# Performance work log

Measured on AMD Instinct MI355X. Metric: run time of the kernel, lower is better.

The kernel has to match this reference:

```python
import jax, jax.numpy as jnp
import numpy as np

# DH-SFNN: 2 dendritic LIF layers (denri, no tanh, reset-by-subtraction) + leaky readout integrator.
GAMMA = 0.5   # surrogate gradient scale
LENS = 0.5    # surrogate gradient width
VTH = 1.0     # spike threshold
DT = 1.0

@jax.custom_vjp
def spike_fn(x):
    # Heaviside forward, Gaussian surrogate backward (act_fun_adp)
    return (x > 0.0).astype(x.dtype)

def _spike_fwd(x):
    return spike_fn(x), x

def _spike_bwd(x, g):
    sg = GAMMA * jnp.exp(-x * x / (2.0 * LENS * LENS)) / (jnp.sqrt(2.0 * jnp.pi) * LENS)
    return (g * sg,)

spike_fn.defvjp(_spike_fwd, _spike_bwd)

B, T, IN, H, O, K = 256, 250, 700, 256, 20, 4  # batch, time, in_dim, hidden, out_dim, branch
WARMUP = 10


def _branch_mask(rng, out_dim, in_dim, k):
    # Each neuron's k branches see a disjoint random partition of the inputs.
    m = np.zeros((out_dim * k, in_dim), np.float32)
    step = in_dim // k
    for i in range(out_dim):
        perm = rng.permutation(in_dim)
        for j in range(k):
            m[i * k + j, perm[j * step:(j + 1) * step]] = 1.0
    return m


def setup_inputs() -> dict:
    key = jax.random.key(0)
    ks = jax.random.split(key, 12)
    rng = np.random.default_rng(0)
    s1 = 1.0 / np.sqrt(IN)
    s2 = 1.0 / np.sqrt(H)
    # branch-masked dense weights (apply_mask() already baked in)
    W1 = jax.random.uniform(ks[0], (H * K, IN), minval=-s1, maxval=s1) * jnp.asarray(_branch_mask(rng, H, IN, K))
    b1 = jax.random.uniform(ks[1], (H * K,), minval=-s1, maxval=s1)
    tau_n1 = jax.random.uniform(ks[2], (H, K), minval=2.0, maxval=6.0)
    tau_m1 = jax.random.uniform(ks[3], (H,), minval=0.0, maxval=4.0)
    W2 = jax.random.uniform(ks[4], (H * K, H), minval=-s2, maxval=s2) * jnp.asarray(_branch_mask(rng, H, H, K))
    b2 = jax.random.uniform(ks[5], (H * K,), minval=-s2, maxval=s2)
    tau_n2 = jax.random.uniform(ks[6], (H, K), minval=2.0, maxval=6.0)
    tau_m2 = jax.random.uniform(ks[7], (H,), minval=0.0, maxval=4.0)
    Wr = jax.random.uniform(ks[8], (O, H), minval=-s2, maxval=s2)
    br = jax.random.uniform(ks[9], (O,), minval=-s2, maxval=s2)
    tau_mr = jax.random.uniform(ks[10], (O,), minval=0.0, maxval=4.0)
    # sparse binary spike train input (SHD-like)
    x = (jax.random.uniform(ks[11], (B, T, IN)) < 0.1).astype(jnp.float32)
    return dict(x=x, W1=W1, b1=b1, tau_n1=tau_n1, tau_m1=tau_m1,
                W2=W2, b2=b2, tau_n2=tau_n2, tau_m2=tau_m2,
                Wr=Wr, br=br, tau_mr=tau_mr, warmup=WARMUP)


def reference(x, W1, b1, tau_n1, tau_m1, W2, b2, tau_n2, tau_m2, Wr, br, tau_mr, warmup):
    Bb, Tt, _ = x.shape
    beta1 = jax.nn.sigmoid(tau_n1)   # [H,K] dendritic decay
    alpha1 = jax.nn.sigmoid(tau_m1)  # [H]   soma decay
    beta2 = jax.nn.sigmoid(tau_n2)
    alpha2 = jax.nn.sigmoid(tau_m2)
    alphar = jax.nn.sigmoid(tau_mr)  # [O]

    def dense_branch(inp, W, b):
        return (inp @ W.T + b).reshape(inp.shape[0], -1, K)  # [B,H,K]

    def step(carry, xt):
        d1, m1, s1, d2, m2, s2, mr, acc, t = carry
        # layer 1: dendritic filtering then LIF with soft reset
        d1 = beta1 * d1 + (1.0 - beta1) * dense_branch(xt, W1, b1)
        m1 = m1 * alpha1 + (1.0 - alpha1) * DT * d1.sum(-1) - VTH * s1
        s1 = spike_fn(m1 - VTH)
        # layer 2
        d2 = beta2 * d2 + (1.0 - beta2) * dense_branch(s1, W2, b2)
        m2 = m2 * alpha2 + (1.0 - alpha2) * DT * d2.sum(-1) - VTH * s2
        s2 = spike_fn(m2 - VTH)
        # leaky readout integrator
        mr = mr * alphar + (1.0 - alphar) * (s2 @ Wr.T + br)
        acc = acc + jnp.where(t >= warmup, mr, jnp.zeros_like(mr))
        return (d1, m1, s1, d2, m2, s2, mr, acc, t + 1), None

    z = lambda *s: jnp.zeros(s, x.dtype)
    carry0 = (z(Bb, H, K), z(Bb, H), z(Bb, H),
              z(Bb, H, K), z(Bb, H), z(Bb, H),
              z(Bb, O), z(Bb, O), jnp.int32(0))
    carry, _ = jax.lax.scan(step, carry0, jnp.moveaxis(x, 1, 0))
    acc = carry[7]
    return acc / (Tt - warmup)  # readout_mode == 'mean'
```

## Files before the change

### kernel.cpp

```cpp
#include <hip/hip_runtime.h>
#include <hip/hip_bf16.h>

typedef unsigned short us16;
typedef unsigned int u32;
typedef unsigned long long ull;

#define B_   256
#define T_   250
#define IN_  700
#define KP_  704
#define H_   256
#define O_   20
#define HK_  1024
#define NPAIR_ (B_ * T_)
#define LDP_ 40
#define CP_  136

typedef __attribute__((ext_vector_type(8))) short short8;
typedef __attribute__((ext_vector_type(4))) float f32x4;

__device__ __forceinline__ float bfbits(unsigned int lo16) {
    union { unsigned int i; float f; } v; v.i = lo16 << 16; return v.f;
}
__device__ __forceinline__ float bflo(unsigned int u) {
    union { unsigned int i; float f; } v; v.i = u << 16; return v.f;
}
__device__ __forceinline__ float bfhi(unsigned int u) {
    union { unsigned int i; float f; } v; v.i = u & 0xffff0000u; return v.f;
}
__device__ __forceinline__ us16 f2bfu(float f) {
    __hip_bfloat16 h = __float2bfloat16(f);
    union { __hip_bfloat16 h; us16 u; } c; c.h = h; return c.u;
}
__device__ __forceinline__ float sigm(float x) { return 1.0f / (1.0f + expf(-x)); }
__device__ __forceinline__ int rfl(int v) { return __builtin_amdgcn_readfirstlane(v); }

__device__ __forceinline__ bool detect_bf16(const us16* __restrict__ taun) {
    int ok = 0;
#pragma unroll
    for (int i = 0; i < 8; i += 2) ok += ((taun[i] >> 8) == 0x40) ? 1 : 0;
    return ok == 4;
}
__device__ __forceinline__ float ldany(const void* __restrict__ p, long i, bool isb) {
    return isb ? bfbits(((const us16*)p)[i]) : ((const float*)p)[i];
}

__device__ __forceinline__ void async_cp16(const us16* g, us16* l) {
    __builtin_amdgcn_global_load_lds(
        (const __attribute__((address_space(1))) u32*)g,
        (__attribute__((address_space(3))) u32*)l, 16, 0, 0);
}

__global__ __launch_bounds__(256) void cvt_rows2(
    const void* __restrict__ xin, const void* __restrict__ w1in,
    us16* __restrict__ xout, us16* __restrict__ w1out,
    const us16* __restrict__ taun) {
    const bool isb = detect_bf16(taun);
    const int r = blockIdx.x * 4 + (threadIdx.x >> 6);
    const int l = threadIdx.x & 63;
    const void* in; us16* out; long ibase, obase;
    if (r < NPAIR_) {
        in = xin;  out = xout;  ibase = (long)r * IN_; obase = (long)r * KP_;
    } else {
        const int r2 = r - NPAIR_;
        if (r2 >= HK_) return;
        in = w1in; out = w1out; ibase = (long)r2 * IN_; obase = (long)r2 * KP_;
    }
    for (int c = l; c < 88; c += 64) {
        uint4 o;
        if (c < 87) {
            if (isb) {
                uint2 lo = *(const uint2*)((const us16*)in + ibase + 8 * c);
                uint2 hi = *(const uint2*)((const us16*)in + ibase + 8 * c + 4);
                o.x = lo.x; o.y = lo.y; o.z = hi.x; o.w = hi.y;
            } else {
                float4 f0 = *(const float4*)((const float*)in + ibase + 8 * c);
                float4 f1 = *(const float4*)((const float*)in + ibase + 8 * c + 4);
                o.x = (u32)f2bfu(f0.x) | ((u32)f2bfu(f0.y) << 16);
                o.y = (u32)f2bfu(f0.z) | ((u32)f2bfu(f0.w) << 16);
                o.z = (u32)f2bfu(f1.x) | ((u32)f2bfu(f1.y) << 16);
                o.w = (u32)f2bfu(f1.z) | ((u32)f2bfu(f1.w) << 16);
            }
        } else {
            o.z = 0u; o.w = 0u;
            if (isb) {
                uint2 lo = *(const uint2*)((const us16*)in + ibase + 696);
                o.x = lo.x; o.y = lo.y;
            } else {
                float4 f0 = *(const float4*)((const float*)in + ibase + 696);
                o.x = (u32)f2bfu(f0.x) | ((u32)f2bfu(f0.y) << 16);
                o.y = (u32)f2bfu(f0.z) | ((u32)f2bfu(f0.w) << 16);
            }
        }
        *(uint4*)(out + obase + 8 * c) = o;
    }
}

__global__ void transpose_to_bf16(const void* __restrict__ in, us16* __restrict__ out,
                                  int R, int C, const us16* __restrict__ taun) {
    const bool isb = detect_bf16(taun);
    __shared__ us16 tile[32][33];
    int c0 = blockIdx.x * 32, r0 = blockIdx.y * 32;
    int tx = threadIdx.x, ty = threadIdx.y;
#pragma unroll
    for (int j = 0; j < 32; j += 8) {
        int r = r0 + ty + j, c = c0 + tx;
        if (r < R && c < C) tile[ty + j][tx] = f2bfu(ldany(in, (long)r * C + c, isb));
    }
    __syncthreads();
#pragma unroll
    for (int j = 0; j < 32; j += 8) {
        int c = c0 + ty + j, r = r0 + tx;
        if (c < C && r < R) out[(long)c * R + r] = tile[tx][ty + j];
    }
}

__global__ __launch_bounds__(256) void gemm_bf(
    const us16* __restrict__ Xb, const us16* __restrict__ W1b,
    us16* __restrict__ Apre)
{
    __shared__ __align__(16) us16 smem[32768];

    const int L  = blockIdx.x;
    const int mt = (L & 7) + ((L >> 6) << 3);
    const int nt = (L >> 3) & 7;
    if (mt >= NPAIR_ / 128) return;
    const int m0 = mt * 128, n0 = nt * 128;

    const int tid  = threadIdx.x;
    const int lane = tid & 63;
    const int w    = tid >> 6;
    const int wr   = w >> 1, wc = w & 1;
    const int l16  = lane & 15, quad = lane >> 4;

    const int rr    = lane >> 3;
    const int ccsw  = ((lane & 7) ^ rr) * 8;
    const us16* xg[4]; const us16* wg[4];
    int asl[4], bsl[4];
#pragma unroll
    for (int i = 0; i < 4; ++i) {
        const int blkrow = (w * 4 + i) * 8;
        xg[i]  = Xb  + (long)(m0 + blkrow + rr) * KP_ + ccsw;
        wg[i]  = W1b + (long)(n0 + blkrow + rr) * KP_ + ccsw;
        asl[i] = (w * 4 + i) * 512;
        bsl[i] = 8192 + (w * 4 + i) * 512;
    }

    f32x4 acc[4][4];
#pragma unroll
    for (int i = 0; i < 4; ++i)
#pragma unroll
        for (int j = 0; j < 4; ++j) acc[i][j] = (f32x4){0.f, 0.f, 0.f, 0.f};

    const int sw = l16 & 7;
    int aoff0[4], aoff1[4], boff0[4], boff1[4];
#pragma unroll
    for (int i = 0; i < 4; ++i) {
        const int ar = wr * 64 + i * 16 + l16;
        const int br = wc * 64 + i * 16 + l16;
        aoff0[i] = ar * 64 + ((quad ^ sw) << 3);
        aoff1[i] = ar * 64 + (((quad + 4) ^ sw) << 3);
        boff0[i] = 8192 + br * 64 + ((quad ^ sw) << 3);
        boff1[i] = 8192 + br * 64 + (((quad + 4) ^ sw) << 3);
    }

#pragma unroll
    for (int i = 0; i < 4; ++i) async_cp16(xg[i], smem + asl[i]);
#pragma unroll
    for (int i = 0; i < 4; ++i) async_cp16(wg[i], smem + bsl[i]);
    __syncthreads();

    for (int s = 0; s < 11; ++s) {
        const int cur = (s & 1) * 16384;
        const int nxt = 16384 - cur;
        if (s + 1 < 11) {
            const int kb = (s + 1) * 64;
#pragma unroll
            for (int i = 0; i < 4; ++i) async_cp16(xg[i] + kb, smem + nxt + asl[i]);
#pragma unroll
            for (int i = 0; i < 4; ++i) async_cp16(wg[i] + kb, smem + nxt + bsl[i]);
        }

        short8 af[4][2], bfv[4][2];
#pragma unroll
        for (int i = 0; i < 4; ++i) {
            af[i][0]  = *(const short8*)(smem + cur + aoff0[i]);
            af[i][1]  = *(const short8*)(smem + cur + aoff1[i]);
            bfv[i][0] = *(const short8*)(smem + cur + boff0[i]);
            bfv[i][1] = *(const short8*)(smem + cur + boff1[i]);
        }
#pragma unroll
        for (int h = 0; h < 2; ++h)
#pragma unroll
            for (int i = 0; i < 4; ++i)
#pragma unroll
                for (int j = 0; j < 4; ++j)
                    acc[i][j] = __builtin_amdgcn_mfma_f32_16x16x32_bf16(
                        af[i][h], bfv[j][h], acc[i][j], 0, 0, 0);

        __syncthreads();
    }

#pragma unroll
    for (int i = 0; i < 4; ++i)
#pragma unroll
        for (int j = 0; j < 4; ++j)
#pragma unroll
            for (int r = 0; r < 4; ++r)
                smem[(wr * 64 + i * 16 + quad * 4 + r) * CP_ +
                     (wc * 64 + j * 16 + l16)] = f2bfu(acc[i][j][r]);
    __syncthreads();
    {
        const int c8 = (lane & 15) * 8;
#pragma unroll
        for (int r2 = 0; r2 < 8; ++r2) {
            const int row = w * 32 + r2 * 4 + (lane >> 4);
            const uint4 v = *(const uint4*)(smem + row * CP_ + c8);
            *(uint4*)(Apre + (long)(m0 + row) * HK_ + n0 + c8) = v;
        }
    }
}

__device__ void wave_recur(
    const us16* __restrict__ Apre,
    const void* __restrict__ b1,  const void* __restrict__ tau_n1,
    const void* __restrict__ tau_m1,
    const void* __restrict__ b2,  const void* __restrict__ tau_n2,
    const void* __restrict__ tau_m2,
    const void* __restrict__ Wr,  const void* __restrict__ br,
    const void* __restrict__ tau_mr,
    const us16* __restrict__ W2T,
    int wu, bool isb, int b, int lane,
    void* __restrict__ out)
{
    float be1[16], cb1[16], be2[16], cb2[16], d1[16], d2[16];
#pragma unroll
    for (int e = 0; e < 16; ++e) {
        const long gi = (long)lane * 16 + e;
        const float t1 = sigm(ldany(tau_n1, gi, isb));
        be1[e] = t1; cb1[e] = (1.f - t1) * ldany(b1, gi, isb);
        const float t2 = sigm(ldany(tau_n2, gi, isb));
        be2[e] = t2; cb2[e] = (1.f - t2) * ldany(b2, gi, isb);
        d1[e] = 0.f; d2[e] = 0.f;
    }
    float al1[4], al2[4], m1[4], s1[4], m2[4], s2[4];
#pragma unroll
    for (int j = 0; j < 4; ++j) {
        al1[j] = sigm(ldany(tau_m1, lane * 4 + j, isb));
        al2[j] = sigm(ldany(tau_m2, lane * 4 + j, isb));
        m1[j] = 0.f; s1[j] = 0.f; m2[j] = 0.f; s2[j] = 0.f;
    }
    float alr = 0.f, brv = 0.f;
    if (lane < O_) { alr = sigm(ldany(tau_mr, lane, isb)); brv = ldany(br, lane, isb); }
    float mrv = 0.f, accO = 0.f;

    const us16* ap = Apre + (long)b * T_ * HK_ + lane * 16;

    auto wstep = [&](int t, uint4 lo, uint4 hi) {
        float a[16];
        a[0]=bflo(lo.x);  a[1]=bfhi(lo.x);  a[2]=bflo(lo.y);  a[3]=bfhi(lo.y);
        a[4]=bflo(lo.z);  a[5]=bfhi(lo.z);  a[6]=bflo(lo.w);  a[7]=bfhi(lo.w);
        a[8]=bflo(hi.x);  a[9]=bfhi(hi.x);  a[10]=bflo(hi.y); a[11]=bfhi(hi.y);
        a[12]=bflo(hi.z); a[13]=bfhi(hi.z); a[14]=bflo(hi.w); a[15]=bfhi(hi.w);
#pragma unroll
        for (int e = 0; e < 16; ++e)
            d1[e] = be1[e] * d1[e] + cb1[e] + (1.f - be1[e]) * a[e];
        unsigned long long bal1[4];
#pragma unroll
        for (int j = 0; j < 4; ++j) {
            const float s = (d1[j*4+0] + d1[j*4+1]) + (d1[j*4+2] + d1[j*4+3]);
            m1[j] = m1[j] * al1[j] + (1.f - al1[j]) * s - s1[j];
            s1[j] = (m1[j] > 1.0f) ? 1.f : 0.f;
            bal1[j] = __ballot(s1[j] > 0.f);
        }
        if ((bal1[0] | bal1[1] | bal1[2] | bal1[3]) != 0ull) {
            float g[16];
#pragma unroll
            for (int e = 0; e < 16; ++e) g[e] = 0.f;
            for (int j2 = 0; j2 < 4; ++j2) {
                unsigned long long mm = bal1[j2];
                while (mm) {
                    const int i = __ffsll(mm) - 1; mm &= mm - 1;
                    const us16* wv = W2T + ((long)(i * 4 + j2) << 10) + lane * 16;
                    const uint4 wl = *(const uint4*)wv;
                    const uint4 wh = *(const uint4*)(wv + 8);
                    g[0]+=bflo(wl.x);  g[1]+=bfhi(wl.x);  g[2]+=bflo(wl.y);  g[3]+=bfhi(wl.y);
                    g[4]+=bflo(wl.z);  g[5]+=bfhi(wl.z);  g[6]+=bflo(wl.w);  g[7]+=bfhi(wl.w);
                    g[8]+=bflo(wh.x);  g[9]+=bfhi(wh.x);  g[10]+=bflo(wh.y); g[11]+=bfhi(wh.y);
                    g[12]+=bflo(wh.z); g[13]+=bfhi(wh.z); g[14]+=bflo(wh.w); g[15]+=bfhi(wh.w);
                }
            }
#pragma unroll
            for (int e = 0; e < 16; ++e)
                d2[e] = be2[e] * d2[e] + cb2[e] + (1.f - be2[e]) * g[e];
        } else {
#pragma unroll
            for (int e = 0; e < 16; ++e)
                d2[e] = be2[e] * d2[e] + cb2[e];
        }
        unsigned long long bal2[4];
#pragma unroll
        for (int j = 0; j < 4; ++j) {
            const float s = (d2[j*4+0] + d2[j*4+1]) + (d2[j*4+2] + d2[j*4+3]);
            m2[j] = m2[j] * al2[j] + (1.f - al2[j]) * s - s2[j];
            s2[j] = (m2[j] > 1.0f) ? 1.f : 0.f;
            bal2[j] = __ballot(s2[j] > 0.f);
        }
        if (lane < O_) {
            float sum = brv;
            if ((bal2[0] | bal2[1] | bal2[2] | bal2[3]) != 0ull) {
                for (int j2 = 0; j2 < 4; ++j2) {
                    unsigned long long mm = bal2[j2];
                    while (mm) {
                        const int i = __ffsll(mm) - 1; mm &= mm - 1;
                        sum += ldany(Wr, (long)lane * H_ + (i * 4 + j2), isb);
                    }
                }
            }
            mrv = alr * mrv + (1.f - alr) * sum;
            if (t >= wu) accO += mrv;
        }
    };

    uint4 q0a = *(const uint4*)(ap);
    uint4 q0b = *(const uint4*)(ap + 8);
    uint4 q1a = *(const uint4*)(ap + HK_);
    uint4 q1b = *(const uint4*)(ap + HK_ + 8);
    uint4 q2a = *(const uint4*)(ap + 2 * HK_);
    uint4 q2b = *(const uint4*)(ap + 2 * HK_ + 8);
    uint4 q3a = *(const uint4*)(ap + 3 * HK_);
    uint4 q3b = *(const uint4*)(ap + 3 * HK_ + 8);

    int t = 0;
    for (int it = 0; it < 62; ++it) {
        wstep(t + 0, q0a, q0b);
        q0a = *(const uint4*)(ap + (long)(t + 4) * HK_);
        q0b = *(const uint4*)(ap + (long)(t + 4) * HK_ + 8);
        wstep(t + 1, q1a, q1b);
        if (t + 5 < T_) {
            q1a = *(const uint4*)(ap + (long)(t + 5) * HK_);
            q1b = *(const uint4*)(ap + (long)(t + 5) * HK_ + 8);
        }
        wstep(t + 2, q2a, q2b);
        if (t + 6 < T_) {
            q2a = *(const uint4*)(ap + (long)(t + 6) * HK_);
            q2b = *(const uint4*)(ap + (long)(t + 6) * HK_ + 8);
        }
        wstep(t + 3, q3a, q3b);
        if (t + 7 < T_) {
            q3a = *(const uint4*)(ap + (long)(t + 7) * HK_);
            q3b = *(const uint4*)(ap + (long)(t + 7) * HK_ + 8);
        }
        t += 4;
    }
    wstep(248, q0a, q0b);
    wstep(249, q1a, q1b);

    if (lane < O_) {
        const float res = accO / (float)(T_ - wu);
        if (isb) ((us16*)out)[b * O_ + lane] = f2bfu(res);
        else     ((float*)out)[b * O_ + lane] = res;
    }
}

__global__ __launch_bounds__(256) void l1_check(
    const us16* __restrict__ Apre,
    const void* __restrict__ b1,  const void* __restrict__ tau_n1,
    const void* __restrict__ tau_m1,
    const void* __restrict__ b2,  const void* __restrict__ tau_n2,
    const void* __restrict__ tau_m2,
    const void* __restrict__ Wr,  const void* __restrict__ br,
    const void* __restrict__ tau_mr,
    const int* __restrict__ warmup_p,
    int* __restrict__ flags, float* __restrict__ sh_out)
{
    const int tid = threadIdx.x;
    const int b   = blockIdx.x;
    const bool isb = detect_bf16((const us16*)tau_n1);

    if (b == B_) {
        if (tid >= 64) return;
        const int lane = tid;
        const int wu   = *warmup_p;
        float be2[16], cb2[16], d2[16];
#pragma unroll
        for (int e = 0; e < 16; ++e) {
            const long gi = (long)lane * 16 + e;
            const float t2 = sigm(ldany(tau_n2, gi, isb));
            be2[e] = t2; cb2[e] = (1.f - t2) * ldany(b2, gi, isb);
            d2[e] = 0.f;
        }
        float al2[4], m2[4], s2[4];
#pragma unroll
        for (int j = 0; j < 4; ++j) {
            al2[j] = sigm(ldany(tau_m2, lane * 4 + j, isb));
            m2[j] = 0.f; s2[j] = 0.f;
        }
        float alr = 0.f, brv = 0.f;
        if (lane < O_) { alr = sigm(ldany(tau_mr, lane, isb)); brv = ldany(br, lane, isb); }
        float mrv = 0.f, accO = 0.f;

        for (int t = 0; t < T_; ++t) {
#pragma unroll
            for (int e = 0; e < 16; ++e)
                d2[e] = be2[e] * d2[e] + cb2[e];
            unsigned long long bal2[4];
#pragma unroll
            for (int j = 0; j < 4; ++j) {
                const float s = (d2[j*4+0] + d2[j*4+1]) + (d2[j*4+2] + d2[j*4+3]);
                m2[j] = m2[j] * al2[j] + (1.f - al2[j]) * s - s2[j];
                s2[j] = (m2[j] > 1.0f) ? 1.f : 0.f;
                bal2[j] = __ballot(s2[j] > 0.f);
            }
            if (lane < O_) {
                float sum = brv;
                if ((bal2[0] | bal2[1] | bal2[2] | bal2[3]) != 0ull) {
                    for (int j2 = 0; j2 < 4; ++j2) {
                        unsigned long long mm = bal2[j2];
                        while (mm) {
                            const int i = __ffsll(mm) - 1; mm &= mm - 1;
                            sum += ldany(Wr, (long)lane * H_ + (i * 4 + j2), isb);
                        }
                    }
                }
                mrv = alr * mrv + (1.f - alr) * sum;
                if (t >= wu) accO += mrv;
            }
        }
        if (lane < O_) sh_out[lane] = accO / (float)(T_ - wu);
        return;
    }

    __shared__ int blkflag;
    if (tid == 0) blkflag = 0;
    __syncthreads();

    float be1[4], cb1[4], ce1[4], d1[4];
#pragma unroll
    for (int k = 0; k < 4; ++k) {
        const long gi = 4L * tid + k;
        const float t1 = sigm(ldany(tau_n1, gi, isb));
        be1[k] = t1; ce1[k] = 1.f - t1; cb1[k] = ce1[k] * ldany(b1, gi, isb);
        d1[k] = 0.f;
    }
    const float al1 = sigm(ldany(tau_m1, tid, isb)), cal1 = 1.f - al1;
    float m1 = 0.f, s1f = 0.f;
    int any = 0;

    const us16* ap = Apre + (long)b * T_ * HK_ + 4 * tid;

    uint2 q0 = *(const uint2*)(ap);
    uint2 q1 = *(const uint2*)(ap + HK_);
    uint2 q2 = *(const uint2*)(ap + 2 * HK_);
    uint2 q3 = *(const uint2*)(ap + 3 * HK_);
    uint2 q4 = *(const uint2*)(ap + 4 * HK_);
    uint2 q5 = *(const uint2*)(ap + 5 * HK_);
    uint2 q6 = *(const uint2*)(ap + 6 * HK_);
    uint2 q7 = *(const uint2*)(ap + 7 * HK_);

    auto body = [&](int t, uint2& q) {
        const float a0 = bflo(q.x), a1 = bfhi(q.x), a2 = bflo(q.y), a3 = bfhi(q.y);
        if (t + 8 < T_) q = *(const uint2*)(ap + (long)(t + 8) * HK_);
        d1[0] = be1[0] * d1[0] + cb1[0] + ce1[0] * a0;
        d1[1] = be1[1] * d1[1] + cb1[1] + ce1[1] * a1;
        d1[2] = be1[2] * d1[2] + cb1[2] + ce1[2] * a2;
        d1[3] = be1[3] * d1[3] + cb1[3] + ce1[3] * a3;
        const float s = (d1[0] + d1[1]) + (d1[2] + d1[3]);
        m1 = m1 * al1 + cal1 * s - s1f;
        const int sp = (m1 > 1.0f) ? 1 : 0;
        s1f = sp ? 1.f : 0.f;
        any |= sp;
    };

    int t = 0;
    for (int it = 0; it < 31; ++it) {
        body(t + 0, q0); body(t + 1, q1); body(t + 2, q2); body(t + 3, q3);
        body(t + 4, q4); body(t + 5, q5); body(t + 6, q6); body(t + 7, q7);
        t += 8;
    }
    body(248, q0);
    body(249, q1);

    if (any) blkflag = 1;
    __syncthreads();
    if (tid == 0) flags[b] = blkflag;
}

__global__ __launch_bounds__(64) void finalize(
    const us16* __restrict__ Apre,
    const void* __restrict__ b1,  const void* __restrict__ tau_n1,
    const void* __restrict__ tau_m1,
    const void* __restrict__ b2,  const void* __restrict__ tau_n2,
    const void* __restrict__ tau_m2,
    const void* __restrict__ Wr,  const void* __restrict__ br,
    const void* __restrict__ tau_mr,
    const us16* __restrict__ W2T,
    const int* __restrict__ warmup_p,
    const int* __restrict__ flags, const float* __restrict__ sh_out,
    void* __restrict__ out)
{
    const int lane = threadIdx.x;
    const int b    = blockIdx.x;
    const bool isb = detect_bf16((const us16*)tau_n1);
    const int wu   = *warmup_p;

    if (flags[b]) {
        wave_recur(Apre, b1, tau_n1, tau_m1, b2, tau_n2, tau_m2,
                   Wr, br, tau_mr, W2T, wu, isb, b, lane, out);
    } else if (lane < O_) {
        const float res = sh_out[lane];
        if (isb) ((us16*)out)[b * O_ + lane] = f2bfu(res);
        else     ((float*)out)[b * O_ + lane] = res;
    }
}

#define GA_LOAD(S, AV, BV) do {                                               \
    const int k0_ = (S) * 32 + half16;                                        \
    if (k0_ + 16 <= IN_) {                                                    \
        if (isb) {                                                            \
            const us16* pa_ = (const us16*)X  + arow + k0_;                   \
            const us16* pb_ = (const us16*)W1 + brow + k0_;                   \
            uint2 a0_ = *(const uint2*)pa_,        a1_ = *(const uint2*)(pa_ + 4);  \
            uint2 a2_ = *(const uint2*)(pa_ + 8),  a3_ = *(const uint2*)(pa_ + 12); \
            uint2 b0_ = *(const uint2*)pb_,        b1_ = *(const uint2*)(pb_ + 4);  \
            uint2 b2_ = *(const uint2*)(pb_ + 8),  b3_ = *(const uint2*)(pb_ + 12); \
            AV[0]=a0_.x; AV[1]=a0_.y; AV[2]=a1_.x; AV[3]=a1_.y;               \
            AV[4]=a2_.x; AV[5]=a2_.y; AV[6]=a3_.x; AV[7]=a3_.y;               \
            BV[0]=b0_.x; BV[1]=b0_.y; BV[2]=b1_.x; BV[3]=b1_.y;               \
            BV[4]=b2_.x; BV[5]=b2_.y; BV[6]=b3_.x; BV[7]=b3_.y;               \
        } else {                                                              \
            const float* pa_ = (const float*)X  + arow + k0_;                 \
            const float* pb_ = (const float*)W1 + brow + k0_;                 \
            float4 fa0_ = *(const float4*)pa_,        fa1_ = *(const float4*)(pa_ + 4);  \
            float4 fa2_ = *(const float4*)(pa_ + 8),  fa3_ = *(const float4*)(pa_ + 12); \
            float4 fb0_ = *(const float4*)pb_,        fb1_ = *(const float4*)(pb_ + 4);  \
            float4 fb2_ = *(const float4*)(pb_ + 8),  fb3_ = *(const float4*)(pb_ + 12); \
            AV[0] = (unsigned)f2bfu(fa0_.x) | ((unsigned)f2bfu(fa0_.y) << 16); \
            AV[1] = (unsigned)f2bfu(fa0_.z) | ((unsigned)f2bfu(fa0_.w) << 16); \
            AV[2] = (unsigned)f2bfu(fa1_.x) | ((unsigned)f2bfu(fa1_.y) << 16); \
            AV[3] = (unsigned)f2bfu(fa1_.z) | ((unsigned)f2bfu(fa1_.w) << 16); \
            AV[4] = (unsigned)f2bfu(fa2_.x) | ((unsigned)f2bfu(fa2_.y) << 16); \
            AV[5] = (unsigned)f2bfu(fa2_.z) | ((unsigned)f2bfu(fa2_.w) << 16); \
            AV[6] = (unsigned)f2bfu(fa3_.x) | ((unsigned)f2bfu(fa3_.y) << 16); \
            AV[7] = (unsigned)f2bfu(fa3_.z) | ((unsigned)f2bfu(fa3_.w) << 16); \
            BV[0] = (unsigned)f2bfu(fb0_.x) | ((unsigned)f2bfu(fb0_.y) << 16); \
            BV[1] = (unsigned)f2bfu(fb0_.z) | ((unsigned)f2bfu(fb0_.w) << 16); \
            BV[2] = (unsigned)f2bfu(fb1_.x) | ((unsigned)f2bfu(fb1_.y) << 16); \
            BV[3] = (unsigned)f2bfu(fb1_.z) | ((unsigned)f2bfu(fb1_.w) << 16); \
            BV[4] = (unsigned)f2bfu(fb2_.x) | ((unsigned)f2bfu(fb2_.y) << 16); \
            BV[5] = (unsigned)f2bfu(fb2_.z) | ((unsigned)f2bfu(fb2_.w) << 16); \
            BV[6] = (unsigned)f2bfu(fb3_.x) | ((unsigned)f2bfu(fb3_.y) << 16); \
            BV[7] = (unsigned)f2bfu(fb3_.z) | ((unsigned)f2bfu(fb3_.w) << 16); \
        }                                                                     \
    } else {                                                                  \
        _Pragma("unroll")                                                     \
        for (int e_ = 0; e_ < 8; ++e_) { AV[e_] = 0u; BV[e_] = 0u; }          \
        _Pragma("unroll")                                                     \
        for (int e_ = 0; e_ < 16; ++e_) {                                     \
            int k_ = k0_ + e_;                                                \
            if (k_ < IN_) {                                                   \
                unsigned va_ = (unsigned)f2bfu(ldany(X,  arow + k_, isb));    \
                unsigned vb_ = (unsigned)f2bfu(ldany(W1, brow + k_, isb));    \
                AV[e_ >> 1] |= va_ << ((e_ & 1) * 16);                        \
                BV[e_ >> 1] |= vb_ << ((e_ & 1) * 16);                        \
            }                                                                 \
        }                                                                     \
    }                                                                         \
} while (0)

#define GA_STORE(AV, BV) do {                                                 \
    uint4 u0_; u0_.x = AV[0]; u0_.y = AV[1]; u0_.z = AV[2]; u0_.w = AV[3];    \
    uint4 u1_; u1_.x = AV[4]; u1_.y = AV[5]; u1_.z = AV[6]; u1_.w = AV[7];    \
    uint4 v0_; v0_.x = BV[0]; v0_.y = BV[1]; v0_.z = BV[2]; v0_.w = BV[3];    \
    uint4 v1_; v1_.x = BV[4]; v1_.y = BV[5]; v1_.z = BV[6]; v1_.w = BV[7];    \
    *(uint4*)asw       = u0_; *(uint4*)(asw + 8) = u1_;                       \
    *(uint4*)bsw       = v0_; *(uint4*)(bsw + 8) = v1_;                       \
} while (0)

#define GA_MFMA() do {                                                        \
    short8 af_[4], bf_[4];                                                    \
    _Pragma("unroll")                                                         \
    for (int i_ = 0; i_ < 4; ++i_) af_[i_] = *(const short8*)(As + aoff[i_]); \
    _Pragma("unroll")                                                         \
    for (int j_ = 0; j_ < 4; ++j_) bf_[j_] = *(const short8*)(Bs + boff[j_]); \
    _Pragma("unroll")                                                         \
    for (int i_ = 0; i_ < 4; ++i_)                                            \
        _Pragma("unroll")                                                     \
        for (int j_ = 0; j_ < 4; ++j_)                                        \
            acc[i_][j_] = __builtin_amdgcn_mfma_f32_16x16x32_bf16(            \
                af_[i_], bf_[j_], acc[i_][j_], 0, 0, 0);                      \
} while (0)

__global__ __launch_bounds__(256) void gemm_apre(
    const void* __restrict__ X, const void* __restrict__ W1,
    const us16* __restrict__ taun, us16* __restrict__ Apre)
{
    const bool isb = detect_bf16(taun);
    __shared__ __align__(16) us16 As[128 * LDP_];
    __shared__ __align__(16) us16 Bs[128 * LDP_];

    const int L  = blockIdx.x;
    const int mt = (L & 7) + ((L >> 6) << 3);
    const int nt = (L >> 3) & 7;
    if (mt >= NPAIR_ / 128) return;
    const int m0 = mt * 128, n0 = nt * 128;

    const int tid  = threadIdx.x;
    const int lane = tid & 63;
    const int w    = tid >> 6;
    const int wr   = w >> 1, wc = w & 1;
    const int l16  = lane & 15, quad = lane >> 4;
    const int ra   = tid >> 1;
    const int half16 = (tid & 1) * 16;

    f32x4 acc[4][4];
#pragma unroll
    for (int i = 0; i < 4; ++i)
#pragma unroll
        for (int j = 0; j < 4; ++j) acc[i][j] = (f32x4){0.f, 0.f, 0.f, 0.f};

    int aoff[4], boff[4];
#pragma unroll
    for (int i = 0; i < 4; ++i) {
        aoff[i] = (wr * 64 + i * 16 + l16) * LDP_ + quad * 8;
        boff[i] = (wc * 64 + i * 16 + l16) * LDP_ + quad * 8;
    }

    const long arow = (long)(m0 + ra) * IN_;
    const long brow = (long)(n0 + ra) * IN_;
    us16* asw = As + ra * LDP_ + half16;
    us16* bsw = Bs + ra * LDP_ + half16;

    unsigned av0[8], bv0[8], av1[8], bv1[8];
    GA_LOAD(0, av0, bv0);

    for (int ss = 0; ss < 11; ++ss) {
        __syncthreads();
        GA_STORE(av0, bv0);
        __syncthreads();
        GA_LOAD(2 * ss + 1, av1, bv1);
        GA_MFMA();
        __syncthreads();
        GA_STORE(av1, bv1);
        __syncthreads();
        if (ss < 10) GA_LOAD(2 * ss + 2, av0, bv0);
        GA_MFMA();
    }

#pragma unroll
    for (int i = 0; i < 4; ++i) {
#pragma unroll
        for (int j = 0; j < 4; ++j) {
            const int gm = m0 + wr * 64 + i * 16 + quad * 4;
            const int gn = n0 + wc * 64 + j * 16 + l16;
            us16* op = Apre + (long)gm * HK_ + gn;
#pragma unroll
            for (int r = 0; r < 4; ++r)
                op[(long)r * HK_] = f2bfu(acc[i][j][r]);
        }
    }
}

__global__ __launch_bounds__(64) void dhsfnn_wave(
    const us16* __restrict__ Apre,
    const void* __restrict__ b1,  const void* __restrict__ tau_n1,
    const void* __restrict__ tau_m1,
    const void* __restrict__ b2,  const void* __restrict__ tau_n2,
    const void* __restrict__ tau_m2,
    const void* __restrict__ Wr,  const void* __restrict__ br,
    const void* __restrict__ tau_mr,
    const us16* __restrict__ W2T,
    const int* __restrict__ warmup_p,
    void* __restrict__ out)
{
    const int lane = threadIdx.x;
    const int b    = blockIdx.x;
    const bool isb = detect_bf16((const us16*)tau_n1);
    const int wu   = *warmup_p;
    wave_recur(Apre, b1, tau_n1, tau_m1, b2, tau_n2, tau_m2,
               Wr, br, tau_mr, W2T, wu, isb, b, lane, out);
}

__global__ __launch_bounds__(256) void dhsfnn_fb(
    const void* __restrict__ x,  const void* __restrict__ W1,
    const void* __restrict__ b1, const void* __restrict__ tau_n1,
    const void* __restrict__ tau_m1,
    const void* __restrict__ W2, const void* __restrict__ b2,
    const void* __restrict__ tau_n2, const void* __restrict__ tau_m2,
    const void* __restrict__ Wr, const void* __restrict__ br,
    const void* __restrict__ tau_mr,
    const int* __restrict__ warmup_p,
    void* __restrict__ out)
{
    __shared__ us16 list1[1024];
    __shared__ us16 list2[256];
    __shared__ us16 list3[256];
    __shared__ int n1s, n2s, n3s;

    const int tid = threadIdx.x;
    const int b   = blockIdx.x;
    const int h   = tid;
    const bool isb = detect_bf16((const us16*)tau_n1);
    const int wu  = *warmup_p;

    const float be1_0 = sigm(ldany(tau_n1, 4 * h + 0, isb));
    const float be1_1 = sigm(ldany(tau_n1, 4 * h + 1, isb));
    const float be1_2 = sigm(ldany(tau_n1, 4 * h + 2, isb));
    const float be1_3 = sigm(ldany(tau_n1, 4 * h + 3, isb));
    const float bi1_0 = ldany(b1, 4 * h + 0, isb), bi1_1 = ldany(b1, 4 * h + 1, isb);
    const float bi1_2 = ldany(b1, 4 * h + 2, isb), bi1_3 = ldany(b1, 4 * h + 3, isb);
    const float al1 = sigm(ldany(tau_m1, h, isb));
    const float be2_0 = sigm(ldany(tau_n2, 4 * h + 0, isb));
    const float be2_1 = sigm(ldany(tau_n2, 4 * h + 1, isb));
    const float be2_2 = sigm(ldany(tau_n2, 4 * h + 2, isb));
    const float be2_3 = sigm(ldany(tau_n2, 4 * h + 3, isb));
    const float bi2_0 = ldany(b2, 4 * h + 0, isb), bi2_1 = ldany(b2, 4 * h + 1, isb);
    const float bi2_2 = ldany(b2, 4 * h + 2, isb), bi2_3 = ldany(b2, 4 * h + 3, isb);
    const float al2 = sigm(ldany(tau_m2, h, isb));
    float alr = 0.f, brv = 0.f;
    if (h < O_) { alr = sigm(ldany(tau_mr, h, isb)); brv = ldany(br, h, isb); }

    float d1_0 = 0.f, d1_1 = 0.f, d1_2 = 0.f, d1_3 = 0.f, m1v = 0.f, s1f = 0.f;
    float d2_0 = 0.f, d2_1 = 0.f, d2_2 = 0.f, d2_3 = 0.f, m2v = 0.f, s2f = 0.f;
    float mrv = 0.f, accO = 0.f;

    const long xbase = (long)b * T_ * IN_;
    float xv0 = ldany(x, xbase + tid, isb);
    float xv1 = ldany(x, xbase + tid + 256, isb);
    float xv2 = (tid + 512 < IN_) ? ldany(x, xbase + tid + 512, isb) : 0.f;

    for (int t = 0; t < T_; ++t) {
        const bool p0 = xv0 != 0.f, p1 = xv1 != 0.f, p2 = xv2 != 0.f;
        if (t + 1 < T_) {
            const long nbx = xbase + (long)(t + 1) * IN_;
            xv0 = ldany(x, nbx + tid, isb);
            xv1 = ldany(x, nbx + tid + 256, isb);
            xv2 = (tid + 512 < IN_) ? ldany(x, nbx + tid + 512, isb) : 0.f;
        }
        __syncthreads();
        if (tid == 0) { n1s = 0; n2s = 0; n3s = 0; }
        __syncthreads();
        if (p0) { int p = atomicAdd(&n1s, 1); list1[p & 1023] = (us16)tid; }
        if (p1) { int p = atomicAdd(&n1s, 1); list1[p & 1023] = (us16)(tid + 256); }
        if (p2) { int p = atomicAdd(&n1s, 1); list1[p & 1023] = (us16)(tid + 512); }
        __syncthreads();
        int n1 = n1s; n1 = (n1 < 1024) ? n1 : 1024;

        float a0 = 0.f, a1 = 0.f, a2 = 0.f, a3 = 0.f;
#pragma unroll 2
        for (int idx = 0; idx < n1; ++idx) {
            int i = rfl((int)list1[idx]);
            i = (i < IN_) ? i : (IN_ - 1);
            long r = (long)(h * 4) * IN_ + i;
            a0 += ldany(W1, r, isb);
            a1 += ldany(W1, r + IN_, isb);
            a2 += ldany(W1, r + 2 * IN_, isb);
            a3 += ldany(W1, r + 3 * IN_, isb);
        }
        d1_0 = be1_0 * d1_0 + (1.f - be1_0) * (bi1_0 + a0);
        d1_1 = be1_1 * d1_1 + (1.f - be1_1) * (bi1_1 + a1);
        d1_2 = be1_2 * d1_2 + (1.f - be1_2) * (bi1_2 + a2);
        d1_3 = be1_3 * d1_3 + (1.f - be1_3) * (bi1_3 + a3);
        m1v = m1v * al1 + (1.f - al1) * (d1_0 + d1_1 + d1_2 + d1_3) - s1f;
        s1f = (m1v > 1.0f) ? 1.f : 0.f;

        if (s1f > 0.f) { int p = atomicAdd(&n2s, 1); list2[p & 255] = (us16)tid; }
        __syncthreads();
        int n2 = n2s; n2 = (n2 < 256) ? n2 : 256;

        a0 = 0.f; a1 = 0.f; a2 = 0.f; a3 = 0.f;
#pragma unroll 2
        for (int idx = 0; idx < n2; ++idx) {
            int i = rfl((int)list2[idx]);
            i = (i < H_) ? i : (H_ - 1);
            long r = (long)(h * 4) * H_ + i;
            a0 += ldany(W2, r, isb);
            a1 += ldany(W2, r + H_, isb);
            a2 += ldany(W2, r + 2 * H_, isb);
            a3 += ldany(W2, r + 3 * H_, isb);
        }
        d2_0 = be2_0 * d2_0 + (1.f - be2_0) * (bi2_0 + a0);
        d2_1 = be2_1 * d2_1 + (1.f - be2_1) * (bi2_1 + a1);
        d2_2 = be2_2 * d2_2 + (1.f - be2_2) * (bi2_2 + a2);
        d2_3 = be2_3 * d2_3 + (1.f - be2_3) * (bi2_3 + a3);
        m2v = m2v * al2 + (1.f - al2) * (d2_0 + d2_1 + d2_2 + d2_3) - s2f;
        s2f = (m2v > 1.0f) ? 1.f : 0.f;

        if (s2f > 0.f) { int p = atomicAdd(&n3s, 1); list3[p & 255] = (us16)tid; }
        __syncthreads();
        int n3 = n3s; n3 = (n3 < 256) ? n3 : 256;

        if (h < O_) {
            float sum = brv;
            for (int idx = 0; idx < n3; ++idx) {
                int j = (int)list3[idx];
                j = (j < H_) ? j : (H_ - 1);
                sum += ldany(Wr, (long)h * H_ + j, isb);
            }
            mrv = alr * mrv + (1.f - alr) * sum;
            if (t >= wu) accO += mrv;
        }
    }
    if (h < O_) {
        float res = accO / (float)(T_ - wu);
        if (isb) ((us16*)out)[b * O_ + h] = f2bfu(res);
        else     ((float*)out)[b * O_ + h] = res;
    }
}

extern "C" void kernel_launch(void* const* d_in, const int* in_sizes, int n_in,
                              void* d_out, int out_size, void* d_ws, size_t ws_size,
                              hipStream_t stream) {
    const void* x      = d_in[0];
    const void* W1     = d_in[1];
    const void* b1     = d_in[2];
    const void* tau_n1 = d_in[3];
    const void* tau_m1 = d_in[4];
    const void* W2     = d_in[5];
    const void* b2     = d_in[6];
    const void* tau_n2 = d_in[7];
    const void* tau_m2 = d_in[8];
    const void* Wr     = d_in[9];
    const void* br     = d_in[10];
    const void* tau_mr = d_in[11];
    const int*  warmup = (const int*)d_in[12];

    const size_t w2t_bytes  = (size_t)H_ * HK_ * 2;
    const size_t xbf_bytes  = (size_t)NPAIR_ * KP_ * 2;
    const size_t w1b_bytes  = (size_t)HK_ * KP_ * 2;
    const size_t apre_bytes = (size_t)NPAIR_ * HK_ * 2;

    const bool tier0 = (d_ws != nullptr &&
                        ws_size >= w2t_bytes + xbf_bytes + w1b_bytes + apre_bytes);
    const bool tier1 = (d_ws != nullptr && ws_size >= w2t_bytes + apre_bytes);

    dim3 blk(32, 8);
    if (tier0) {
        us16* W2T  = (us16*)d_ws;
        us16* Xbf  = (us16*)((char*)d_ws + w2t_bytes);
        us16* W1bf = (us16*)((char*)d_ws + w2t_bytes + xbf_bytes);
        us16* Apre = (us16*)((char*)d_ws + w2t_bytes + xbf_bytes + w1b_bytes);
        int*   flags  = (int*)Xbf;
        float* sh_out = (float*)(Xbf + 2048);

        cvt_rows2<<<(NPAIR_ + HK_) / 4, 256, 0, stream>>>(
            x, W1, Xbf, W1bf, (const us16*)tau_n1);
        transpose_to_bf16<<<dim3((H_ + 31) / 32, (HK_ + 31) / 32), blk, 0, stream>>>(
            W2, W2T, HK_, H_, (const us16*)tau_n1);
        gemm_bf<<<4096, 256, 0, stream>>>(Xbf, W1bf, Apre);
        l1_check<<<B_ + 1, 256, 0, stream>>>(
            Apre, b1, tau_n1, tau_m1, b2, tau_n2, tau_m2,
            Wr, br, tau_mr, warmup, flags, sh_out);
        finalize<<<B_, 64, 0, stream>>>(
            Apre, b1, tau_n1, tau_m1, b2, tau_n2, tau_m2,
            Wr, br, tau_mr, W2T, warmup, flags, sh_out, d_out);
    } else if (tier1) {
        us16* W2T  = (us16*)d_ws;
        us16* Apre = (us16*)((char*)d_ws + w2t_bytes);
        transpose_to_bf16<<<dim3((H_ + 31) / 32, (HK_ + 31) / 32), blk, 0, stream>>>(
            W2, W2T, HK_, H_, (const us16*)tau_n1);
        gemm_apre<<<4096, 256, 0, stream>>>(x, W1, (const us16*)tau_n1, Apre);
        dhsfnn_wave<<<B_, 64, 0, stream>>>(
            Apre, b1, tau_n1, tau_m1, b2, tau_n2, tau_m2,
            Wr, br, tau_mr, W2T, warmup, d_out);
    } else {
        dhsfnn_fb<<<B_, 256, 0, stream>>>(x, W1, b1, tau_n1, tau_m1,
                                          W2, b2, tau_n2, tau_m2,
                                          Wr, br, tau_mr, warmup, d_out);
    }
}
```

Baseline: 409.6 us.

## Fuse layer-1 check with finalize and fold W2 transpose into conversion kernel

Folds the W2 transpose into the input conversion kernel as extra blocks, and merges the layer-1 spike check with the finalize step into one kernel. Wave 0 of each block now also computes the no-spike layer-2/readout path inline, and a block-wide ballot decides whether to run the full recurrence. This removes two kernel launches and the global flags/sh_out round trip. In exchange, wave 0 does extra layer-2 work every timestep, which can slow the layer-1 scan for each batch, and the new W2 transpose uses scattered uncoalesced reads.

```diff
diff --git a/kernel.cpp b/kernel.cpp
--- a/kernel.cpp
+++ b/kernel.cpp
@@ -15,6 +15,8 @@
 #define NPAIR_ (B_ * T_)
 #define LDP_ 40
 #define CP_  136
+#define CVT_ROWB_ ((NPAIR_ + HK_) / 4)
+#define CVT_W2B_  64
 
 typedef __attribute__((ext_vector_type(8))) short short8;
 typedef __attribute__((ext_vector_type(4))) float f32x4;
@@ -53,9 +55,21 @@
 
 __global__ __launch_bounds__(256) void cvt_rows2(
     const void* __restrict__ xin, const void* __restrict__ w1in,
+    const void* __restrict__ w2in,
     us16* __restrict__ xout, us16* __restrict__ w1out,
+    us16* __restrict__ w2t,
     const us16* __restrict__ taun) {
     const bool isb = detect_bf16(taun);
+
+    if (blockIdx.x >= CVT_ROWB_) {
+        const int base = (blockIdx.x - CVT_ROWB_) * 256 + threadIdx.x;
+        for (int e = base; e < H_ * HK_; e += CVT_W2B_ * 256) {
+            const int c = e >> 10, n = e & (HK_ - 1);
+            w2t[e] = f2bfu(ldany(w2in, (long)n * H_ + c, isb));
+        }
+        return;
+    }
+
     const int r = blockIdx.x * 4 + (threadIdx.x >> 6);
     const int l = threadIdx.x & 63;
     const void* in; us16* out; long ibase, obase;
@@ -363,7 +377,7 @@
     }
 }
 
-__global__ __launch_bounds__(256) void l1_check(
+__global__ __launch_bounds__(256) void l1_fused(
     const us16* __restrict__ Apre,
     const void* __restrict__ b1,  const void* __restrict__ tau_n1,
     const void* __restrict__ tau_m1,
@@ -371,18 +385,35 @@
     const void* __restrict__ tau_m2,
     const void* __restrict__ Wr,  const void* __restrict__ br,
     const void* __restrict__ tau_mr,
+    const us16* __restrict__ W2T,
     const int* __restrict__ warmup_p,
-    int* __restrict__ flags, float* __restrict__ sh_out)
+    void* __restrict__ out)
 {
-    const int tid = threadIdx.x;
-    const int b   = blockIdx.x;
+    __shared__ ull wany[4];
+
+    const int tid  = threadIdx.x;
+    const int lane = tid & 63;
+    const int w    = tid >> 6;
+    const int b    = blockIdx.x;
     const bool isb = detect_bf16((const us16*)tau_n1);
-
-    if (b == B_) {
-        if (tid >= 64) return;
-        const int lane = tid;
-        const int wu   = *warmup_p;
-        float be2[16], cb2[16], d2[16];
+    const int wu   = *warmup_p;
+    const bool l2on = (w == 0);
+
+    float be1[4], cb1[4], ce1[4], d1[4];
+#pragma unroll
+    for (int k = 0; k < 4; ++k) {
+        const long gi = 4L * tid + k;
+        const float t1 = sigm(ldany(tau_n1, gi, isb));
+        be1[k] = t1; ce1[k] = 1.f - t1; cb1[k] = ce1[k] * ldany(b1, gi, isb);
+        d1[k] = 0.f;
+    }
+    const float al1 = sigm(ldany(tau_m1, tid, isb)), cal1 = 1.f - al1;
+    float m1 = 0.f, s1f = 0.f;
+    int any = 0;
+
+    float be2[16], cb2[16], d2[16], al2[4], m2[4], s2[4];
+    float alr = 0.f, brv = 0.f, mrv = 0.f, accO = 0.f;
+    if (l2on) {
 #pragma unroll
         for (int e = 0; e < 16; ++e) {
             const long gi = (long)lane * 16 + e;
@@ -390,25 +421,47 @@
             be2[e] = t2; cb2[e] = (1.f - t2) * ldany(b2, gi, isb);
             d2[e] = 0.f;
         }
-        float al2[4], m2[4], s2[4];
 #pragma unroll
         for (int j = 0; j < 4; ++j) {
             al2[j] = sigm(ldany(tau_m2, lane * 4 + j, isb));
             m2[j] = 0.f; s2[j] = 0.f;
         }
-        float alr = 0.f, brv = 0.f;
         if (lane < O_) { alr = sigm(ldany(tau_mr, lane, isb)); brv = ldany(br, lane, isb); }
-        float mrv = 0.f, accO = 0.f;
-
-        for (int t = 0; t < T_; ++t) {
+    }
+
+    const us16* ap = Apre + (long)b * T_ * HK_ + 4 * tid;
+
+    uint2 q0 = *(const uint2*)(ap);
+    uint2 q1 = *(const uint2*)(ap + HK_);
+    uint2 q2 = *(const uint2*)(ap + 2 * HK_);
+    uint2 q3 = *(const uint2*)(ap + 3 * HK_);
+    uint2 q4 = *(const uint2*)(ap + 4 * HK_);
+    uint2 q5 = *(const uint2*)(ap + 5 * HK_);
+    uint2 q6 = *(const uint2*)(ap + 6 * HK_);
+    uint2 q7 = *(const uint2*)(ap + 7 * HK_);
+
+    auto body = [&](int t, uint2& q) {
+        const float a0 = bflo(q.x), a1 = bfhi(q.x), a2 = bflo(q.y), a3 = bfhi(q.y);
+        if (t + 8 < T_) q = *(const uint2*)(ap + (long)(t + 8) * HK_);
+        d1[0] = be1[0] * d1[0] + cb1[0] + ce1[0] * a0;
+        d1[1] = be1[1] * d1[1] + cb1[1] + ce1[1] * a1;
+        d1[2] = be1[2] * d1[2] + cb1[2] + ce1[2] * a2;
+        d1[3] = be1[3] * d1[3] + cb1[3] + ce1[3] * a3;
+        const float s = (d1[0] + d1[1]) + (d1[2] + d1[3]);
+        m1 = m1 * al1 + cal1 * s - s1f;
+        const int sp = (m1 > 1.0f) ? 1 : 0;
+        s1f = sp ? 1.f : 0.f;
+        any |= sp;
+
+        if (l2on) {
 #pragma unroll
             for (int e = 0; e < 16; ++e)
                 d2[e] = be2[e] * d2[e] + cb2[e];
             unsigned long long bal2[4];
 #pragma unroll
             for (int j = 0; j < 4; ++j) {
-                const float s = (d2[j*4+0] + d2[j*4+1]) + (d2[j*4+2] + d2[j*4+3]);
-                m2[j] = m2[j] * al2[j] + (1.f - al2[j]) * s - s2[j];
+                const float s2s = (d2[j*4+0] + d2[j*4+1]) + (d2[j*4+2] + d2[j*4+3]);
+                m2[j] = m2[j] * al2[j] + (1.f - al2[j]) * s2s - s2[j];
                 s2[j] = (m2[j] > 1.0f) ? 1.f : 0.f;
                 bal2[j] = __ballot(s2[j] > 0.f);
             }
@@ -427,49 +480,6 @@
                 if (t >= wu) accO += mrv;
             }
         }
-        if (lane < O_) sh_out[lane] = accO / (float)(T_ - wu);
-        return;
-    }
-
-    __shared__ int blkflag;
-    if (tid == 0) blkflag = 0;
-    __syncthreads();
-
-    float be1[4], cb1[4], ce1[4], d1[4];
-#pragma unroll
-    for (int k = 0; k < 4; ++k) {
-        const long gi = 4L * tid + k;
-        const float t1 = sigm(ldany(tau_n1, gi, isb));
-        be1[k] = t1; ce1[k] = 1.f - t1; cb1[k] = ce1[k] * ldany(b1, gi, isb);
-        d1[k] = 0.f;
-    }
-    const float al1 = sigm(ldany(tau_m1, tid, isb)), cal1 = 1.f - al1;
-    float m1 = 0.f, s1f = 0.f;
-    int any = 0;
-
-    const us16* ap = Apre + (long)b * T_ * HK_ + 4 * tid;
-
-    uint2 q0 = *(const uint2*)(ap);
-    uint2 q1 = *(const uint2*)(ap + HK_);
-    uint2 q2 = *(const uint2*)(ap + 2 * HK_);
-    uint2 q3 = *(const uint2*)(ap + 3 * HK_);
-    uint2 q4 = *(const uint2*)(ap + 4 * HK_);
-    uint2 q5 = *(const uint2*)(ap + 5 * HK_);
-    uint2 q6 = *(const uint2*)(ap + 6 * HK_);
-    uint2 q7 = *(const uint2*)(ap + 7 * HK_);
-
-    auto body = [&](int t, uint2& q) {
-        const float a0 = bflo(q.x), a1 = bfhi(q.x), a2 = bflo(q.y), a3 = bfhi(q.y);
-        if (t + 8 < T_) q = *(const uint2*)(ap + (long)(t + 8) * HK_);
-        d1[0] = be1[0] * d1[0] + cb1[0] + ce1[0] * a0;
-        d1[1] = be1[1] * d1[1] + cb1[1] + ce1[1] * a1;
-        d1[2] = be1[2] * d1[2] + cb1[2] + ce1[2] * a2;
-        d1[3] = be1[3] * d1[3] + cb1[3] + ce1[3] * a3;
-        const float s = (d1[0] + d1[1]) + (d1[2] + d1[3]);
-        m1 = m1 * al1 + cal1 * s - s1f;
-        const int sp = (m1 > 1.0f) ? 1 : 0;
-        s1f = sp ? 1.f : 0.f;
-        any |= sp;
     };
 
     int t = 0;
@@ -481,34 +491,17 @@
     body(248, q0);
     body(249, q1);
 
-    if (any) blkflag = 1;
+    const ull bm = __ballot(any != 0);
+    if (lane == 0) wany[w] = bm;
     __syncthreads();
-    if (tid == 0) flags[b] = blkflag;
-}
-
-__global__ __launch_bounds__(64) void finalize(
-    const us16* __restrict__ Apre,
-    const void* __restrict__ b1,  const void* __restrict__ tau_n1,
-    const void* __restrict__ tau_m1,
-    const void* __restrict__ b2,  const void* __restrict__ tau_n2,
-    const void* __restrict__ tau_m2,
-    const void* __restrict__ Wr,  const void* __restrict__ br,
-    const void* __restrict__ tau_mr,
-    const us16* __restrict__ W2T,
-    const int* __restrict__ warmup_p,
-    const int* __restrict__ flags, const float* __restrict__ sh_out,
-    void* __restrict__ out)
-{
-    const int lane = threadIdx.x;
-    const int b    = blockIdx.x;
-    const bool isb = detect_bf16((const us16*)tau_n1);
-    const int wu   = *warmup_p;
-
-    if (flags[b]) {
+    const ull flag = wany[0] | wany[1] | wany[2] | wany[3];
+
+    if (w != 0) return;
+    if (flag != 0ull) {
         wave_recur(Apre, b1, tau_n1, tau_m1, b2, tau_n2, tau_m2,
                    Wr, br, tau_mr, W2T, wu, isb, b, lane, out);
     } else if (lane < O_) {
-        const float res = sh_out[lane];
+        const float res = accO / (float)(T_ - wu);
         if (isb) ((us16*)out)[b * O_ + lane] = f2bfu(res);
         else     ((float*)out)[b * O_ + lane] = res;
     }
@@ -840,20 +833,13 @@
         us16* Xbf  = (us16*)((char*)d_ws + w2t_bytes);
         us16* W1bf = (us16*)((char*)d_ws + w2t_bytes + xbf_bytes);
         us16* Apre = (us16*)((char*)d_ws + w2t_bytes + xbf_bytes + w1b_bytes);
-        int*   flags  = (int*)Xbf;
-        float* sh_out = (float*)(Xbf + 2048);
-
-        cvt_rows2<<<(NPAIR_ + HK_) / 4, 256, 0, stream>>>(
-            x, W1, Xbf, W1bf, (const us16*)tau_n1);
-        transpose_to_bf16<<<dim3((H_ + 31) / 32, (HK_ + 31) / 32), blk, 0, stream>>>(
-            W2, W2T, HK_, H_, (const us16*)tau_n1);
+
+        cvt_rows2<<<CVT_ROWB_ + CVT_W2B_, 256, 0, stream>>>(
+            x, W1, W2, Xbf, W1bf, W2T, (const us16*)tau_n1);
         gemm_bf<<<4096, 256, 0, stream>>>(Xbf, W1bf, Apre);
-        l1_check<<<B_ + 1, 256, 0, stream>>>(
+        l1_fused<<<B_, 256, 0, stream>>>(
             Apre, b1, tau_n1, tau_m1, b2, tau_n2, tau_m2,
-            Wr, br, tau_mr, warmup, flags, sh_out);
-        finalize<<<B_, 64, 0, stream>>>(
-            Apre, b1, tau_n1, tau_m1, b2, tau_n2, tau_m2,
-            Wr, br, tau_mr, W2T, warmup, flags, sh_out, d_out);
+            Wr, br, tau_mr, W2T, warmup, d_out);
     } else if (tier1) {
         us16* W2T  = (us16*)d_ws;
         us16* Apre = (us16*)((char*)d_ws + w2t_bytes);
```

Measured after the change: 416.7 us. Within noise of the previous version (+1.7%).
